# Optimization experiments

Measured on AMD Instinct MI355X. Metric: run time of the kernel, lower is better.

## Reference

```python
import jax, jax.numpy as jnp
import numpy as np

N_NODES = 50000
N_EDGES = 600000
F_IN = 128
DIM_H = 256
N_CLASSES = 40
BN_EPS = 1e-5


def setup_inputs() -> dict:
    key = jax.random.key(0)
    ks = jax.random.split(key, 10)
    x = jax.random.normal(ks[0], (N_NODES, F_IN), dtype=jnp.float32)
    edge_index = jax.random.randint(ks[1], (2, N_EDGES), 0, N_NODES, dtype=jnp.int64)
    s1 = 1.0 / np.sqrt(F_IN)
    s2 = 1.0 / np.sqrt(DIM_H)
    W1 = jax.random.uniform(ks[2], (F_IN, DIM_H), jnp.float32, -s1, s1)
    b1 = jax.random.uniform(ks[3], (DIM_H,), jnp.float32, -s1, s1)
    gamma = jnp.ones((DIM_H,), jnp.float32)
    beta = jnp.zeros((DIM_H,), jnp.float32)
    W2 = jax.random.uniform(ks[4], (DIM_H, DIM_H), jnp.float32, -s2, s2)
    b2 = jax.random.uniform(ks[5], (DIM_H,), jnp.float32, -s2, s2)
    Wlin = jax.random.uniform(ks[6], (DIM_H, N_CLASSES), jnp.float32, -s2, s2)
    blin = jax.random.uniform(ks[7], (N_CLASSES,), jnp.float32, -s2, s2)
    return {"x": x, "edge_index": edge_index, "W1": W1, "b1": b1,
            "gamma": gamma, "beta": beta, "W2": W2, "b2": b2,
            "Wlin": Wlin, "blin": blin}


def reference(x, edge_index, W1, b1, gamma, beta, W2, b2, Wlin, blin):
    src, dst = edge_index[0], edge_index[1]
    # GIN sum aggregation: agg[i] = sum_{(j->i)} x[j]; eps = 0 (default)
    agg = jax.ops.segment_sum(x[src], dst, num_segments=N_NODES)  # [N, F_IN]
    h = x + agg
    # MLP: Linear -> BatchNorm1d (training-mode batch stats) -> ReLU -> Linear -> ReLU
    h = h @ W1 + b1                               # [N, DIM_H]
    mean = jnp.mean(h, axis=0)
    var = jnp.var(h, axis=0)                      # biased, as torch BN uses for normalization
    h = (h - mean) * jax.lax.rsqrt(var + BN_EPS) * gamma + beta
    h = jax.nn.relu(h)
    h = jax.nn.relu(h @ W2 + b2)                  # MLP final ReLU; outer x.relu() is idempotent
    return h @ Wlin + blin                        # [N, N_CLASSES]
```

## Files before the change

kernel.cpp:

```cpp
#include <hip/hip_runtime.h>

#define F_IN 128
#define DIM_H 256
#define N_CLASSES 40
#define BN_EPS 1e-5f
#define M_PAD 50176

typedef short bf16x8 __attribute__((ext_vector_type(8)));
typedef float f32x4 __attribute__((ext_vector_type(4)));

__device__ __forceinline__ unsigned short f2bf(float f) {
    union { float f; unsigned u; } v; v.f = f;
    unsigned r = v.u + 0x7fff + ((v.u >> 16) & 1);
    return (unsigned short)(r >> 16);
}
__device__ __forceinline__ float bf2f(unsigned short u) {
    union { unsigned u; float f; } v; v.u = ((unsigned)u) << 16;
    return v.f;
}
__device__ __forceinline__ float4 bf2f4(ushort4 u) {
    return make_float4(bf2f(u.x), bf2f(u.y), bf2f(u.z), bf2f(u.w));
}

__global__ void hist_kernel(const int* __restrict__ dst, int* __restrict__ hist, int nE) {
    int e = blockIdx.x * blockDim.x + threadIdx.x;
    if (e >= nE) return;
    atomicAdd(&hist[dst[e]], 1);
}

__global__ void scan_blocks_kernel(const int* __restrict__ hist,
                                   int* __restrict__ blockSums, int M) {
    __shared__ int lds[256];
    int t = threadIdx.x;
    int i = blockIdx.x * 256 + t;
    lds[t] = (i < M) ? hist[i] : 0;
    __syncthreads();
    for (int off = 128; off > 0; off >>= 1) {
        if (t < off) lds[t] += lds[t + off];
        __syncthreads();
    }
    if (t == 0) blockSums[blockIdx.x] = lds[0];
}

__global__ void scan_final_kernel(const int* __restrict__ hist,
                                  const int* __restrict__ blockSums,
                                  int* __restrict__ start, int* __restrict__ cursor,
                                  int M, int nE) {
    __shared__ int lds[256];
    int t = threadIdx.x;
    lds[t] = (t < blockIdx.x) ? blockSums[t] : 0;
    __syncthreads();
    for (int o = 128; o > 0; o >>= 1) {
        if (t < o) lds[t] += lds[t + o];
        __syncthreads();
    }
    int off = lds[0];
    __syncthreads();
    int i = blockIdx.x * 256 + t;
    int orig = (i < M) ? hist[i] : 0;
    lds[t] = orig;
    __syncthreads();
    for (int o = 1; o < 256; o <<= 1) {
        int v = (t >= o) ? lds[t - o] : 0;
        __syncthreads();
        lds[t] += v;
        __syncthreads();
    }
    if (i < M) {
        int v = off + lds[t] - orig;
        start[i] = v;
        cursor[i] = v;
    }
    if (blockIdx.x == 0 && t == 0) start[M] = nE;
}

__global__ void fill_kernel(const int* __restrict__ src, const int* __restrict__ dst,
                            int* __restrict__ cursor,
                            int* __restrict__ order, int nE) {
    int e = blockIdx.x * blockDim.x + threadIdx.x;
    if (e >= nE) return;
    int pos = atomicAdd(&cursor[dst[e]], 1);
    order[pos] = src[e];
}

__global__ void prep_kernel(const float* __restrict__ x, unsigned short* __restrict__ xb,
                            const float* __restrict__ W1, const float* __restrict__ W2,
                            const float* __restrict__ Wl,
                            unsigned short* __restrict__ W1t,
                            unsigned short* __restrict__ W2t,
                            unsigned short* __restrict__ Wlt,
                            int* __restrict__ histz, int XQ, int ZQ) {
    int idx = blockIdx.x * 256 + threadIdx.x;
    if (idx < XQ) {
        float4 v = ((const float4*)x)[idx];
        ushort4 o;
        o.x = f2bf(v.x); o.y = f2bf(v.y); o.z = f2bf(v.z); o.w = f2bf(v.w);
        ((ushort4*)xb)[idx] = o;
        return;
    }
    int j = idx - XQ;
    if (j < 32768) {
        int n = j >> 7, k = j & 127;
        W1t[j] = f2bf(W1[k * DIM_H + n]);
    } else if (j < 32768 + 65536) {
        int i = j - 32768;
        int n = i >> 8, k = i & 255;
        W2t[i] = f2bf(W2[k * DIM_H + n]);
    } else if (j < 32768 + 65536 + 16384) {
        int i = j - 98304;
        int n = i >> 8, k = i & 255;
        Wlt[i] = f2bf((n < N_CLASSES) ? Wl[k * N_CLASSES + n] : 0.f);
    } else {
        int z = j - 114688;
        if (z >= 0 && z < ZQ) ((int4*)histz)[z] = make_int4(0, 0, 0, 0);
    }
}

__global__ void bn_reduce_kernel(const float* __restrict__ partials, int R,
                                 const float* __restrict__ gamma,
                                 const float* __restrict__ beta,
                                 float* __restrict__ scale,
                                 float* __restrict__ shift, int M) {
    __shared__ float ls[256], lss[256];
    int c = blockIdx.x, t = threadIdx.x;
    float s = 0.f, ss = 0.f;
    for (int r = t; r < R; r += 256) {
        s += partials[(long)r * 512 + c];
        ss += partials[(long)r * 512 + 256 + c];
    }
    ls[t] = s; lss[t] = ss;
    __syncthreads();
    for (int o = 128; o > 0; o >>= 1) {
        if (t < o) { ls[t] += ls[t + o]; lss[t] += lss[t + o]; }
        __syncthreads();
    }
    if (t == 0) {
        float inv = 1.0f / (float)M;
        float mean = ls[0] * inv;
        float var = lss[0] * inv - mean * mean;
        float sc = gamma[c] * rsqrtf(var + BN_EPS);
        scale[c] = sc;
        shift[c] = beta[c] - mean * sc;
    }
}

__global__ __launch_bounds__(256) void gather_kernel(
    const unsigned short* __restrict__ xb,
    const int* __restrict__ order, const int* __restrict__ start,
    unsigned short* __restrict__ A1, int M) {
    int node = blockIdx.x * 8 + (threadIdx.x >> 5);
    if (node >= M) return;
    int lane32 = threadIdx.x & 31;
    const ushort4* xv = (const ushort4*)xb;
    float4 a0 = bf2f4(xv[(size_t)node * 32 + lane32]);
    float4 a1 = make_float4(0.f, 0.f, 0.f, 0.f);
    float4 a2 = a1, a3 = a1;
    int e0 = start[node], e1 = start[node + 1];
    int e = e0;
    int c0, c1, c2, c3, c4, c5, c6, c7;
    bool have = (e + 8 <= e1);
    if (have) {
        c0 = order[e];     c1 = order[e + 1]; c2 = order[e + 2]; c3 = order[e + 3];
        c4 = order[e + 4]; c5 = order[e + 5]; c6 = order[e + 6]; c7 = order[e + 7];
    }
    for (; e + 16 <= e1; e += 8) {
        int n0 = order[e + 8],  n1 = order[e + 9],  n2 = order[e + 10], n3 = order[e + 11];
        int n4 = order[e + 12], n5 = order[e + 13], n6 = order[e + 14], n7 = order[e + 15];
        ushort4 u0 = xv[(size_t)c0 * 32 + lane32];
        ushort4 u1 = xv[(size_t)c1 * 32 + lane32];
        ushort4 u2 = xv[(size_t)c2 * 32 + lane32];
        ushort4 u3 = xv[(size_t)c3 * 32 + lane32];
        ushort4 u4 = xv[(size_t)c4 * 32 + lane32];
        ushort4 u5 = xv[(size_t)c5 * 32 + lane32];
        ushort4 u6 = xv[(size_t)c6 * 32 + lane32];
        ushort4 u7 = xv[(size_t)c7 * 32 + lane32];
        float4 v0 = bf2f4(u0), v1 = bf2f4(u1), v2 = bf2f4(u2), v3 = bf2f4(u3);
        float4 v4 = bf2f4(u4), v5 = bf2f4(u5), v6 = bf2f4(u6), v7 = bf2f4(u7);
        a0.x += v0.x; a0.y += v0.y; a0.z += v0.z; a0.w += v0.w;
        a1.x += v1.x; a1.y += v1.y; a1.z += v1.z; a1.w += v1.w;
        a2.x += v2.x; a2.y += v2.y; a2.z += v2.z; a2.w += v2.w;
        a3.x += v3.x; a3.y += v3.y; a3.z += v3.z; a3.w += v3.w;
        a0.x += v4.x; a0.y += v4.y; a0.z += v4.z; a0.w += v4.w;
        a1.x += v5.x; a1.y += v5.y; a1.z += v5.z; a1.w += v5.w;
        a2.x += v6.x; a2.y += v6.y; a2.z += v6.z; a2.w += v6.w;
        a3.x += v7.x; a3.y += v7.y; a3.z += v7.z; a3.w += v7.w;
        c0 = n0; c1 = n1; c2 = n2; c3 = n3; c4 = n4; c5 = n5; c6 = n6; c7 = n7;
    }
    if (have && e + 8 <= e1) {
        ushort4 u0 = xv[(size_t)c0 * 32 + lane32];
        ushort4 u1 = xv[(size_t)c1 * 32 + lane32];
        ushort4 u2 = xv[(size_t)c2 * 32 + lane32];
        ushort4 u3 = xv[(size_t)c3 * 32 + lane32];
        ushort4 u4 = xv[(size_t)c4 * 32 + lane32];
        ushort4 u5 = xv[(size_t)c5 * 32 + lane32];
        ushort4 u6 = xv[(size_t)c6 * 32 + lane32];
        ushort4 u7 = xv[(size_t)c7 * 32 + lane32];
        float4 v0 = bf2f4(u0), v1 = bf2f4(u1), v2 = bf2f4(u2), v3 = bf2f4(u3);
        float4 v4 = bf2f4(u4), v5 = bf2f4(u5), v6 = bf2f4(u6), v7 = bf2f4(u7);
        a0.x += v0.x; a0.y += v0.y; a0.z += v0.z; a0.w += v0.w;
        a1.x += v1.x; a1.y += v1.y; a1.z += v1.z; a1.w += v1.w;
        a2.x += v2.x; a2.y += v2.y; a2.z += v2.z; a2.w += v2.w;
        a3.x += v3.x; a3.y += v3.y; a3.z += v3.z; a3.w += v3.w;
        a0.x += v4.x; a0.y += v4.y; a0.z += v4.z; a0.w += v4.w;
        a1.x += v5.x; a1.y += v5.y; a1.z += v5.z; a1.w += v5.w;
        a2.x += v6.x; a2.y += v6.y; a2.z += v6.z; a2.w += v6.w;
        a3.x += v7.x; a3.y += v7.y; a3.z += v7.z; a3.w += v7.w;
        e += 8;
    }
    for (; e + 4 <= e1; e += 4) {
        int s0 = order[e], s1 = order[e + 1], s2 = order[e + 2], s3 = order[e + 3];
        float4 v0 = bf2f4(xv[(size_t)s0 * 32 + lane32]);
        float4 v1 = bf2f4(xv[(size_t)s1 * 32 + lane32]);
        float4 v2 = bf2f4(xv[(size_t)s2 * 32 + lane32]);
        float4 v3 = bf2f4(xv[(size_t)s3 * 32 + lane32]);
        a0.x += v0.x; a0.y += v0.y; a0.z += v0.z; a0.w += v0.w;
        a1.x += v1.x; a1.y += v1.y; a1.z += v1.z; a1.w += v1.w;
        a2.x += v2.x; a2.y += v2.y; a2.z += v2.z; a2.w += v2.w;
        a3.x += v3.x; a3.y += v3.y; a3.z += v3.z; a3.w += v3.w;
    }
    for (; e < e1; ++e) {
        float4 v = bf2f4(xv[(size_t)order[e] * 32 + lane32]);
        a1.x += v.x; a1.y += v.y; a1.z += v.z; a1.w += v.w;
    }
    float4 t;
    t.x = (a0.x + a1.x) + (a2.x + a3.x);
    t.y = (a0.y + a1.y) + (a2.y + a3.y);
    t.z = (a0.z + a1.z) + (a2.z + a3.z);
    t.w = (a0.w + a1.w) + (a2.w + a3.w);
    ushort4 o;
    o.x = f2bf(t.x); o.y = f2bf(t.y); o.z = f2bf(t.z); o.w = f2bf(t.w);
    ((ushort4*)A1)[(size_t)node * 32 + lane32] = o;
}

__global__ __launch_bounds__(512, 4) void gemm1_kernel(
    const unsigned short* __restrict__ A1, const unsigned short* __restrict__ W1t,
    const float* __restrict__ b1, unsigned short* __restrict__ h1,
    float* __restrict__ partials, int M) {
    constexpr int S = 4;
    constexpr int PA = 40, PB = 40, PH = 264;
    constexpr int STAGE = 128 * PA + 256 * PB;
    __shared__ __align__(16) unsigned short lds[128 * PH];
    unsigned short* h1t = lds;

    int tid = threadIdx.x;
    int wave = tid >> 6, lane = tid & 63;
    int wm = wave >> 2, wn = wave & 3;
    int l15 = lane & 15, q = lane >> 4;
    long row0 = (long)blockIdx.x * 128;

    int am = tid >> 2, ac = tid & 3;
    bf16x8 ar, br[2];
    auto loadAB = [&](int s) {
        ar = *(const bf16x8*)(A1 + (row0 + am) * F_IN + s * 32 + ac * 8);
#pragma unroll
        for (int i = 0; i < 2; ++i) {
            int ch = tid + i * 512;
            int m = ch >> 2, c = ch & 3;
            br[i] = *(const bf16x8*)(W1t + m * F_IN + s * 32 + c * 8);
        }
    };
    auto writeAB = [&](int buf) {
        unsigned short* As = lds + buf * STAGE;
        unsigned short* Bs = As + 128 * PA;
        *(bf16x8*)(&As[am * PA + ac * 8]) = ar;
#pragma unroll
        for (int i = 0; i < 2; ++i) {
            int ch = tid + i * 512;
            int m = ch >> 2, c = ch & 3;
            *(bf16x8*)(&Bs[m * PB + c * 8]) = br[i];
        }
    };

    f32x4 acc[4][4] = {};
    loadAB(0);
    writeAB(0);
#pragma unroll
    for (int s = 0; s < S; ++s) {
        if (s + 1 < S) loadAB(s + 1);
        __syncthreads();
        const unsigned short* As = lds + (s & 1) * STAGE;
        const unsigned short* Bs = As + 128 * PA;
        bf16x8 af[4], bfr[4];
#pragma unroll
        for (int mt = 0; mt < 4; ++mt)
            af[mt] = *(const bf16x8*)(&As[(wm * 64 + mt * 16 + l15) * PA + q * 8]);
#pragma unroll
        for (int nt = 0; nt < 4; ++nt)
            bfr[nt] = *(const bf16x8*)(&Bs[(wn * 64 + nt * 16 + l15) * PB + q * 8]);
#pragma unroll
        for (int mt = 0; mt < 4; ++mt)
#pragma unroll
            for (int nt = 0; nt < 4; ++nt)
                acc[mt][nt] = __builtin_amdgcn_mfma_f32_16x16x32_bf16(
                    af[mt], bfr[nt], acc[mt][nt], 0, 0, 0);
        if (s + 1 < S) writeAB((s + 1) & 1);
    }
    __syncthreads();

#pragma unroll
    for (int nt = 0; nt < 4; ++nt) {
        int col = wn * 64 + nt * 16 + l15;
        float b = b1[col];
        float s = 0.f, ss = 0.f;
#pragma unroll
        for (int mt = 0; mt < 4; ++mt) {
#pragma unroll
            for (int r = 0; r < 4; ++r) {
                long row = row0 + wm * 64 + mt * 16 + q * 4 + r;
                float v = acc[mt][nt][r] + b;
                if (row < M) { s += v; ss += v * v; }
                h1t[(wm * 64 + mt * 16 + q * 4 + r) * PH + col] = f2bf(v);
            }
        }
        s += __shfl_xor(s, 16, 64);  s += __shfl_xor(s, 32, 64);
        ss += __shfl_xor(ss, 16, 64); ss += __shfl_xor(ss, 32, 64);
        if (lane < 16) {
            long pr = (long)blockIdx.x * 2 + wm;
            partials[pr * 512 + col] = s;
            partials[pr * 512 + 256 + col] = ss;
        }
    }
    __syncthreads();
    {
        int srow = tid >> 2, scol = (tid & 3) * 64;
        unsigned short* dst = h1 + (row0 + srow) * DIM_H + scol;
        const unsigned short* srcp = &h1t[srow * PH + scol];
#pragma unroll
        for (int j = 0; j < 8; ++j)
            *(bf16x8*)(dst + j * 8) = *(const bf16x8*)(srcp + j * 8);
    }
}

__global__ __launch_bounds__(512, 4) void gemm23_kernel(
    const unsigned short* __restrict__ h1, const unsigned short* __restrict__ W2t,
    const float* __restrict__ b2,
    const float* __restrict__ scale, const float* __restrict__ shift,
    const unsigned short* __restrict__ Wlt, const float* __restrict__ blin,
    float* __restrict__ out, int M) {
    constexpr int S = 8;
    constexpr int PA = 40, PB = 40, PH = 264;
    constexpr int STAGE = 128 * PA + 256 * PB;
    __shared__ __align__(16) unsigned short lds[128 * PH];
    unsigned short* h2t = lds;

    int tid = threadIdx.x;
    int wave = tid >> 6, lane = tid & 63;
    int wm = wave >> 2, wn = wave & 3;
    int l15 = lane & 15, q = lane >> 4;
    long row0 = (long)blockIdx.x * 128;

    int am = tid >> 2, ac = tid & 3;
    bf16x8 ar, br[2];
    auto loadAB = [&](int s) {
        ar = *(const bf16x8*)(h1 + (row0 + am) * DIM_H + s * 32 + ac * 8);
#pragma unroll
        for (int i = 0; i < 2; ++i) {
            int ch = tid + i * 512;
            int m = ch >> 2, c = ch & 3;
            br[i] = *(const bf16x8*)(W2t + m * DIM_H + s * 32 + c * 8);
        }
    };
    auto writeAB = [&](int s, int buf) {
        unsigned short* As = lds + buf * STAGE;
        unsigned short* Bs = As + 128 * PA;
        {
            int kb = s * 32 + ac * 8;
            float4 sc0 = *(const float4*)(scale + kb);
            float4 sc1 = *(const float4*)(scale + kb + 4);
            float4 sh0 = *(const float4*)(shift + kb);
            float4 sh1 = *(const float4*)(shift + kb + 4);
            float scv[8] = {sc0.x, sc0.y, sc0.z, sc0.w, sc1.x, sc1.y, sc1.z, sc1.w};
            float shv[8] = {sh0.x, sh0.y, sh0.z, sh0.w, sh1.x, sh1.y, sh1.z, sh1.w};
            bf16x8 v = ar;
#pragma unroll
            for (int j = 0; j < 8; ++j) {
                float f = bf2f((unsigned short)v[j]);
                f = fmaxf(f * scv[j] + shv[j], 0.f);
                v[j] = (short)f2bf(f);
            }
            *(bf16x8*)(&As[am * PA + ac * 8]) = v;
        }
#pragma unroll
        for (int i = 0; i < 2; ++i) {
            int ch = tid + i * 512;
            int m = ch >> 2, c = ch & 3;
            *(bf16x8*)(&Bs[m * PB + c * 8]) = br[i];
        }
    };

    f32x4 acc[4][4] = {};
    loadAB(0);
    writeAB(0, 0);
#pragma unroll
    for (int s = 0; s < S; ++s) {
        if (s + 1 < S) loadAB(s + 1);
        __syncthreads();
        const unsigned short* As = lds + (s & 1) * STAGE;
        const unsigned short* Bs = As + 128 * PA;
        bf16x8 af[4], bfr[4];
#pragma unroll
        for (int mt = 0; mt < 4; ++mt)
            af[mt] = *(const bf16x8*)(&As[(wm * 64 + mt * 16 + l15) * PA + q * 8]);
#pragma unroll
        for (int nt = 0; nt < 4; ++nt)
            bfr[nt] = *(const bf16x8*)(&Bs[(wn * 64 + nt * 16 + l15) * PB + q * 8]);
#pragma unroll
        for (int mt = 0; mt < 4; ++mt)
#pragma unroll
            for (int nt = 0; nt < 4; ++nt)
                acc[mt][nt] = __builtin_amdgcn_mfma_f32_16x16x32_bf16(
                    af[mt], bfr[nt], acc[mt][nt], 0, 0, 0);
        if (s + 1 < S) writeAB(s + 1, (s + 1) & 1);
    }
    __syncthreads();

#pragma unroll
    for (int nt = 0; nt < 4; ++nt) {
        int colL = wn * 64 + nt * 16 + l15;
        float b = b2[colL];
#pragma unroll
        for (int mt = 0; mt < 4; ++mt)
#pragma unroll
            for (int r = 0; r < 4; ++r) {
                int rowL = wm * 64 + mt * 16 + q * 4 + r;
                h2t[rowL * PH + colL] = f2bf(fmaxf(acc[mt][nt][r] + b, 0.f));
            }
    }
    __syncthreads();

    f32x4 acc3[3] = {};
#pragma unroll
    for (int s = 0; s < 8; ++s) {
        bf16x8 a3 = *(const bf16x8*)(&h2t[(wave * 16 + l15) * PH + s * 32 + q * 8]);
#pragma unroll
        for (int nt = 0; nt < 3; ++nt) {
            bf16x8 b3 = *(const bf16x8*)(Wlt + (nt * 16 + l15) * 256 + s * 32 + q * 8);
            acc3[nt] = __builtin_amdgcn_mfma_f32_16x16x32_bf16(a3, b3, acc3[nt], 0, 0, 0);
        }
    }
#pragma unroll
    for (int nt = 0; nt < 3; ++nt) {
        int col = nt * 16 + l15;
        if (col < N_CLASSES) {
            float b = blin[col];
#pragma unroll
            for (int r = 0; r < 4; ++r) {
                long row = row0 + wave * 16 + q * 4 + r;
                if (row < M) out[row * N_CLASSES + col] = acc3[nt][r] + b;
            }
        }
    }
}

extern "C" void kernel_launch(void* const* d_in, const int* in_sizes, int n_in,
                              void* d_out, int out_size, void* d_ws, size_t ws_size,
                              hipStream_t stream) {
    const float* x     = (const float*)d_in[0];
    const int*   ei    = (const int*)d_in[1];
    const float* W1    = (const float*)d_in[2];
    const float* b1    = (const float*)d_in[3];
    const float* gamma = (const float*)d_in[4];
    const float* beta  = (const float*)d_in[5];
    const float* W2    = (const float*)d_in[6];
    const float* b2    = (const float*)d_in[7];
    const float* Wlin  = (const float*)d_in[8];
    const float* blin  = (const float*)d_in[9];
    float* out = (float*)d_out;

    int M  = in_sizes[0] / F_IN;
    int nE = in_sizes[1] / 2;
    const int* srcIdx = ei;
    const int* dstIdx = ei + nE;
    int nB = (M + 255) / 256;
    int g128 = (M + 127) / 128;
    int XQ = M * 32;
    int ZQ = M / 4;

    unsigned short* h1bf  = (unsigned short*)d_ws;
    unsigned short* xb    = h1bf + (size_t)M_PAD * DIM_H;
    unsigned short* A1bf  = xb + (size_t)M_PAD * F_IN;
    unsigned short* W1t   = A1bf + (size_t)M_PAD * F_IN;
    unsigned short* W2t   = W1t + DIM_H * F_IN;
    unsigned short* Wlt   = W2t + DIM_H * DIM_H;
    float*          partials = (float*)(Wlt + 64 * DIM_H);
    float*          scale = partials + (size_t)800 * 512;
    float*          shift = scale + DIM_H;
    int*            hist  = (int*)(shift + DIM_H);
    int*            cursor= hist + M;
    int*            start = cursor + M;
    int*            blockSums = start + (M + 1);
    int*            order = blockSums + 256;

    int tB = 256;
    prep_kernel<<<(XQ + 114688 + ZQ + 255) / 256, 256, 0, stream>>>(
        x, xb, W1, W2, Wlin, W1t, W2t, Wlt, hist, XQ, ZQ);
    hist_kernel<<<(nE + tB - 1) / tB, tB, 0, stream>>>(dstIdx, hist, nE);
    scan_blocks_kernel<<<nB, 256, 0, stream>>>(hist, blockSums, M);
    scan_final_kernel<<<nB, 256, 0, stream>>>(hist, blockSums, start, cursor, M, nE);
    fill_kernel<<<(nE + tB - 1) / tB, tB, 0, stream>>>(srcIdx, dstIdx, cursor, order, nE);

    gather_kernel<<<(M + 7) / 8, 256, 0, stream>>>(xb, order, start, A1bf, M);
    gemm1_kernel<<<g128, 512, 0, stream>>>(A1bf, W1t, b1, h1bf, partials, M);
    bn_reduce_kernel<<<DIM_H, 256, 0, stream>>>(partials, 2 * g128, gamma, beta, scale, shift, M);
    gemm23_kernel<<<g128, 512, 0, stream>>>(h1bf, W2t, b2, scale, shift, Wlt, blin, out, M);
}
```

Baseline: 236.2 us.

## Fuse GEMM1, BN reduce and GEMM2/3 into one persistent kernel with grid barriers

Merges gemm1, the BatchNorm reduction and gemm23 into one kernel that keeps the layer-1 accumulators in registers across two software grid barriers. This removes the bf16 h1 round-trip to global memory and two kernel launches. The two-pass scan is also collapsed into one kernel that recomputes each block's prefix by summing all earlier histogram entries. The grid barrier requires all 392 blocks to be co-resident, which holds only if occupancy allows it and risks deadlock otherwise. GEMM2 now reads W2 straight from global memory without LDS staging, and the barrier counters are zeroed through the enlarged histogram clear.

```diff
diff --git a/kernel.cpp b/kernel.cpp
--- a/kernel.cpp
+++ b/kernel.cpp
@@ -22,41 +22,48 @@
     return make_float4(bf2f(u.x), bf2f(u.y), bf2f(u.z), bf2f(u.w));
 }
 
+__device__ __forceinline__ void grid_barrier(int* cnt, int* flag, int nB) {
+    __syncthreads();
+    if (threadIdx.x == 0) {
+        __threadfence();
+        if (atomicAdd(cnt, 1) == nB - 1) {
+            __hip_atomic_store(flag, 1, __ATOMIC_RELEASE, __HIP_MEMORY_SCOPE_AGENT);
+        } else {
+            while (__hip_atomic_load(flag, __ATOMIC_ACQUIRE, __HIP_MEMORY_SCOPE_AGENT) == 0) {
+                __builtin_amdgcn_s_sleep(8);
+            }
+        }
+        __threadfence();
+    }
+    __syncthreads();
+}
+
 __global__ void hist_kernel(const int* __restrict__ dst, int* __restrict__ hist, int nE) {
     int e = blockIdx.x * blockDim.x + threadIdx.x;
     if (e >= nE) return;
     atomicAdd(&hist[dst[e]], 1);
 }
 
-__global__ void scan_blocks_kernel(const int* __restrict__ hist,
-                                   int* __restrict__ blockSums, int M) {
+__global__ void scan_kernel(const int* __restrict__ hist,
+                            int* __restrict__ start, int* __restrict__ cursor,
+                            int M, int nE) {
     __shared__ int lds[256];
+    __shared__ int s_prefix;
     int t = threadIdx.x;
-    int i = blockIdx.x * 256 + t;
-    lds[t] = (i < M) ? hist[i] : 0;
-    __syncthreads();
-    for (int off = 128; off > 0; off >>= 1) {
-        if (t < off) lds[t] += lds[t + off];
-        __syncthreads();
-    }
-    if (t == 0) blockSums[blockIdx.x] = lds[0];
-}
-
-__global__ void scan_final_kernel(const int* __restrict__ hist,
-                                  const int* __restrict__ blockSums,
-                                  int* __restrict__ start, int* __restrict__ cursor,
-                                  int M, int nE) {
-    __shared__ int lds[256];
-    int t = threadIdx.x;
-    lds[t] = (t < blockIdx.x) ? blockSums[t] : 0;
+    int base = blockIdx.x * 256;
+    int s = 0;
+    for (int i = t; i < base; i += 256) s += hist[i];
+    lds[t] = s;
     __syncthreads();
     for (int o = 128; o > 0; o >>= 1) {
         if (t < o) lds[t] += lds[t + o];
         __syncthreads();
     }
-    int off = lds[0];
-    __syncthreads();
-    int i = blockIdx.x * 256 + t;
+    if (t == 0) s_prefix = lds[0];
+    __syncthreads();
+    int prefix = s_prefix;
+    __syncthreads();
+    int i = base + t;
     int orig = (i < M) ? hist[i] : 0;
     lds[t] = orig;
     __syncthreads();
@@ -67,7 +74,7 @@
         __syncthreads();
     }
     if (i < M) {
-        int v = off + lds[t] - orig;
+        int v = prefix + lds[t] - orig;
         start[i] = v;
         cursor[i] = v;
     }
@@ -113,34 +120,6 @@
     } else {
         int z = j - 114688;
         if (z >= 0 && z < ZQ) ((int4*)histz)[z] = make_int4(0, 0, 0, 0);
-    }
-}
-
-__global__ void bn_reduce_kernel(const float* __restrict__ partials, int R,
-                                 const float* __restrict__ gamma,
-                                 const float* __restrict__ beta,
-                                 float* __restrict__ scale,
-                                 float* __restrict__ shift, int M) {
-    __shared__ float ls[256], lss[256];
-    int c = blockIdx.x, t = threadIdx.x;
-    float s = 0.f, ss = 0.f;
-    for (int r = t; r < R; r += 256) {
-        s += partials[(long)r * 512 + c];
-        ss += partials[(long)r * 512 + 256 + c];
-    }
-    ls[t] = s; lss[t] = ss;
-    __syncthreads();
-    for (int o = 128; o > 0; o >>= 1) {
-        if (t < o) { ls[t] += ls[t + o]; lss[t] += lss[t + o]; }
-        __syncthreads();
-    }
-    if (t == 0) {
-        float inv = 1.0f / (float)M;
-        float mean = ls[0] * inv;
-        float var = lss[0] * inv - mean * mean;
-        float sc = gamma[c] * rsqrtf(var + BN_EPS);
-        scale[c] = sc;
-        shift[c] = beta[c] - mean * sc;
     }
 }
 
@@ -232,15 +211,18 @@
     ((ushort4*)A1)[(size_t)node * 32 + lane32] = o;
 }
 
-__global__ __launch_bounds__(512, 4) void gemm1_kernel(
+__global__ __launch_bounds__(512, 4) void mlp_kernel(
     const unsigned short* __restrict__ A1, const unsigned short* __restrict__ W1t,
-    const float* __restrict__ b1, unsigned short* __restrict__ h1,
-    float* __restrict__ partials, int M) {
+    const float* __restrict__ b1,
+    const float* __restrict__ gamma, const float* __restrict__ beta,
+    const unsigned short* __restrict__ W2t, const float* __restrict__ b2,
+    const unsigned short* __restrict__ Wlt, const float* __restrict__ blin,
+    float* __restrict__ partials, float* __restrict__ scale, float* __restrict__ shift,
+    int* __restrict__ bar, float* __restrict__ out, int M, int nB) {
     constexpr int S = 4;
     constexpr int PA = 40, PB = 40, PH = 264;
     constexpr int STAGE = 128 * PA + 256 * PB;
     __shared__ __align__(16) unsigned short lds[128 * PH];
-    unsigned short* h1t = lds;
 
     int tid = threadIdx.x;
     int wave = tid >> 6, lane = tid & 63;
@@ -295,7 +277,6 @@
                     af[mt], bfr[nt], acc[mt][nt], 0, 0, 0);
         if (s + 1 < S) writeAB((s + 1) & 1);
     }
-    __syncthreads();
 
 #pragma unroll
     for (int nt = 0; nt < 4; ++nt) {
@@ -309,7 +290,6 @@
                 long row = row0 + wm * 64 + mt * 16 + q * 4 + r;
                 float v = acc[mt][nt][r] + b;
                 if (row < M) { s += v; ss += v * v; }
-                h1t[(wm * 64 + mt * 16 + q * 4 + r) * PH + col] = f2bf(v);
             }
         }
         s += __shfl_xor(s, 16, 64);  s += __shfl_xor(s, 32, 64);
@@ -320,100 +300,78 @@
             partials[pr * 512 + 256 + col] = ss;
         }
     }
-    __syncthreads();
-    {
-        int srow = tid >> 2, scol = (tid & 3) * 64;
-        unsigned short* dst = h1 + (row0 + srow) * DIM_H + scol;
-        const unsigned short* srcp = &h1t[srow * PH + scol];
-#pragma unroll
-        for (int j = 0; j < 8; ++j)
-            *(bf16x8*)(dst + j * 8) = *(const bf16x8*)(srcp + j * 8);
-    }
-}
-
-__global__ __launch_bounds__(512, 4) void gemm23_kernel(
-    const unsigned short* __restrict__ h1, const unsigned short* __restrict__ W2t,
-    const float* __restrict__ b2,
-    const float* __restrict__ scale, const float* __restrict__ shift,
-    const unsigned short* __restrict__ Wlt, const float* __restrict__ blin,
-    float* __restrict__ out, int M) {
-    constexpr int S = 8;
-    constexpr int PA = 40, PB = 40, PH = 264;
-    constexpr int STAGE = 128 * PA + 256 * PB;
-    __shared__ __align__(16) unsigned short lds[128 * PH];
+
+    grid_barrier(bar, bar + 1, nB);
+
+    if (blockIdx.x < DIM_H) {
+        float* ls = (float*)lds;
+        float* lss = ls + 256;
+        int c = blockIdx.x;
+        int R = 2 * nB;
+        float s = 0.f, ss = 0.f;
+        if (tid < 256) {
+            for (int r = tid; r < R; r += 256) {
+                s += partials[(long)r * 512 + c];
+                ss += partials[(long)r * 512 + 256 + c];
+            }
+            ls[tid] = s; lss[tid] = ss;
+        }
+        __syncthreads();
+        for (int o = 128; o > 0; o >>= 1) {
+            if (tid < o) { ls[tid] += ls[tid + o]; lss[tid] += lss[tid + o]; }
+            __syncthreads();
+        }
+        if (tid == 0) {
+            float inv = 1.0f / (float)M;
+            float mean = ls[0] * inv;
+            float var = lss[0] * inv - mean * mean;
+            float sc = gamma[c] * rsqrtf(var + BN_EPS);
+            scale[c] = sc;
+            shift[c] = beta[c] - mean * sc;
+        }
+    }
+
+    grid_barrier(bar + 2, bar + 3, nB);
+
+    unsigned short* h1t = lds;
+#pragma unroll
+    for (int nt = 0; nt < 4; ++nt) {
+        int col = wn * 64 + nt * 16 + l15;
+        float b = b1[col];
+        float sc = scale[col], sh = shift[col];
+#pragma unroll
+        for (int mt = 0; mt < 4; ++mt) {
+#pragma unroll
+            for (int r = 0; r < 4; ++r) {
+                int rowL = wm * 64 + mt * 16 + q * 4 + r;
+                float v = acc[mt][nt][r] + b;
+                v = fmaxf(v * sc + sh, 0.f);
+                h1t[rowL * PH + col] = f2bf(v);
+            }
+        }
+    }
+    __syncthreads();
+
+    f32x4 acc2[4][4] = {};
+#pragma unroll
+    for (int s = 0; s < 8; ++s) {
+        bf16x8 af[4], bfr[4];
+#pragma unroll
+        for (int mt = 0; mt < 4; ++mt)
+            af[mt] = *(const bf16x8*)(&h1t[(wm * 64 + mt * 16 + l15) * PH + s * 32 + q * 8]);
+#pragma unroll
+        for (int nt = 0; nt < 4; ++nt)
+            bfr[nt] = *(const bf16x8*)(W2t + (wn * 64 + nt * 16 + l15) * DIM_H + s * 32 + q * 8);
+#pragma unroll
+        for (int mt = 0; mt < 4; ++mt)
+#pragma unroll
+            for (int nt = 0; nt < 4; ++nt)
+                acc2[mt][nt] = __builtin_amdgcn_mfma_f32_16x16x32_bf16(
+                    af[mt], bfr[nt], acc2[mt][nt], 0, 0, 0);
+    }
+    __syncthreads();
+
     unsigned short* h2t = lds;
-
-    int tid = threadIdx.x;
-    int wave = tid >> 6, lane = tid & 63;
-    int wm = wave >> 2, wn = wave & 3;
-    int l15 = lane & 15, q = lane >> 4;
-    long row0 = (long)blockIdx.x * 128;
-
-    int am = tid >> 2, ac = tid & 3;
-    bf16x8 ar, br[2];
-    auto loadAB = [&](int s) {
-        ar = *(const bf16x8*)(h1 + (row0 + am) * DIM_H + s * 32 + ac * 8);
-#pragma unroll
-        for (int i = 0; i < 2; ++i) {
-            int ch = tid + i * 512;
-            int m = ch >> 2, c = ch & 3;
-            br[i] = *(const bf16x8*)(W2t + m * DIM_H + s * 32 + c * 8);
-        }
-    };
-    auto writeAB = [&](int s, int buf) {
-        unsigned short* As = lds + buf * STAGE;
-        unsigned short* Bs = As + 128 * PA;
-        {
-            int kb = s * 32 + ac * 8;
-            float4 sc0 = *(const float4*)(scale + kb);
-            float4 sc1 = *(const float4*)(scale + kb + 4);
-            float4 sh0 = *(const float4*)(shift + kb);
-            float4 sh1 = *(const float4*)(shift + kb + 4);
-            float scv[8] = {sc0.x, sc0.y, sc0.z, sc0.w, sc1.x, sc1.y, sc1.z, sc1.w};
-            float shv[8] = {sh0.x, sh0.y, sh0.z, sh0.w, sh1.x, sh1.y, sh1.z, sh1.w};
-            bf16x8 v = ar;
-#pragma unroll
-            for (int j = 0; j < 8; ++j) {
-                float f = bf2f((unsigned short)v[j]);
-                f = fmaxf(f * scv[j] + shv[j], 0.f);
-                v[j] = (short)f2bf(f);
-            }
-            *(bf16x8*)(&As[am * PA + ac * 8]) = v;
-        }
-#pragma unroll
-        for (int i = 0; i < 2; ++i) {
-            int ch = tid + i * 512;
-            int m = ch >> 2, c = ch & 3;
-            *(bf16x8*)(&Bs[m * PB + c * 8]) = br[i];
-        }
-    };
-
-    f32x4 acc[4][4] = {};
-    loadAB(0);
-    writeAB(0, 0);
-#pragma unroll
-    for (int s = 0; s < S; ++s) {
-        if (s + 1 < S) loadAB(s + 1);
-        __syncthreads();
-        const unsigned short* As = lds + (s & 1) * STAGE;
-        const unsigned short* Bs = As + 128 * PA;
-        bf16x8 af[4], bfr[4];
-#pragma unroll
-        for (int mt = 0; mt < 4; ++mt)
-            af[mt] = *(const bf16x8*)(&As[(wm * 64 + mt * 16 + l15) * PA + q * 8]);
-#pragma unroll
-        for (int nt = 0; nt < 4; ++nt)
-            bfr[nt] = *(const bf16x8*)(&Bs[(wn * 64 + nt * 16 + l15) * PB + q * 8]);
-#pragma unroll
-        for (int mt = 0; mt < 4; ++mt)
-#pragma unroll
-            for (int nt = 0; nt < 4; ++nt)
-                acc[mt][nt] = __builtin_amdgcn_mfma_f32_16x16x32_bf16(
-                    af[mt], bfr[nt], acc[mt][nt], 0, 0, 0);
-        if (s + 1 < S) writeAB(s + 1, (s + 1) & 1);
-    }
-    __syncthreads();
-
 #pragma unroll
     for (int nt = 0; nt < 4; ++nt) {
         int colL = wn * 64 + nt * 16 + l15;
@@ -423,7 +381,7 @@
 #pragma unroll
             for (int r = 0; r < 4; ++r) {
                 int rowL = wm * 64 + mt * 16 + q * 4 + r;
-                h2t[rowL * PH + colL] = f2bf(fmaxf(acc[mt][nt][r] + b, 0.f));
+                h2t[rowL * PH + colL] = f2bf(fmaxf(acc2[mt][nt][r] + b, 0.f));
             }
     }
     __syncthreads();
@@ -474,10 +432,9 @@
     int nB = (M + 255) / 256;
     int g128 = (M + 127) / 128;
     int XQ = M * 32;
-    int ZQ = M / 4;
-
-    unsigned short* h1bf  = (unsigned short*)d_ws;
-    unsigned short* xb    = h1bf + (size_t)M_PAD * DIM_H;
+    int ZQ = (M + 4) / 4;
+
+    unsigned short* xb    = (unsigned short*)d_ws;
     unsigned short* A1bf  = xb + (size_t)M_PAD * F_IN;
     unsigned short* W1t   = A1bf + (size_t)M_PAD * F_IN;
     unsigned short* W2t   = W1t + DIM_H * F_IN;
@@ -486,21 +443,20 @@
     float*          scale = partials + (size_t)800 * 512;
     float*          shift = scale + DIM_H;
     int*            hist  = (int*)(shift + DIM_H);
-    int*            cursor= hist + M;
+    int*            bar   = hist + M;
+    int*            cursor= bar + 4;
     int*            start = cursor + M;
-    int*            blockSums = start + (M + 1);
-    int*            order = blockSums + 256;
+    int*            order = start + (M + 1);
 
     int tB = 256;
     prep_kernel<<<(XQ + 114688 + ZQ + 255) / 256, 256, 0, stream>>>(
         x, xb, W1, W2, Wlin, W1t, W2t, Wlt, hist, XQ, ZQ);
     hist_kernel<<<(nE + tB - 1) / tB, tB, 0, stream>>>(dstIdx, hist, nE);
-    scan_blocks_kernel<<<nB, 256, 0, stream>>>(hist, blockSums, M);
-    scan_final_kernel<<<nB, 256, 0, stream>>>(hist, blockSums, start, cursor, M, nE);
+    scan_kernel<<<nB, 256, 0, stream>>>(hist, start, cursor, M, nE);
     fill_kernel<<<(nE + tB - 1) / tB, tB, 0, stream>>>(srcIdx, dstIdx, cursor, order, nE);
 
     gather_kernel<<<(M + 7) / 8, 256, 0, stream>>>(xb, order, start, A1bf, M);
-    gemm1_kernel<<<g128, 512, 0, stream>>>(A1bf, W1t, b1, h1bf, partials, M);
-    bn_reduce_kernel<<<DIM_H, 256, 0, stream>>>(partials, 2 * g128, gamma, beta, scale, shift, M);
-    gemm23_kernel<<<g128, 512, 0, stream>>>(h1bf, W2t, b2, scale, shift, Wlt, blin, out, M);
-}
+    mlp_kernel<<<g128, 512, 0, stream>>>(A1bf, W1t, b1, gamma, beta, W2t, b2,
+                                         Wlt, blin, partials, scale, shift,
+                                         bar, out, M, g128);
+}
```

Result: slower. 351.7 us (+48.9%).
